# Kernel tuning notes

Hardware: AMD Instinct MI355X
Metric: run time of the kernel (lower is better)

Reference implementation:

```python
import jax, jax.numpy as jnp
import numpy as np

R = 131072   # rays
S = 128      # existing samples per ray (existing_bins has S+1 edges)
N_NEW = 64   # new importance samples per ray
HIST_PAD = 1e-5   # NeuSSampler builds PDFSampler(histogram_padding=1e-5)
EPS = 1e-5


def setup_inputs() -> dict:
    key = jax.random.key(0)
    k1, k2, k3, k4 = jax.random.split(key, 4)
    weights = jax.random.uniform(k1, (R, S, 1), dtype=jnp.float32)
    # existing spacing bins must be sorted in [0,1] along the sample axis
    existing_bins = jnp.sort(jax.random.uniform(k2, (R, S + 1), dtype=jnp.float32), axis=-1)
    nears = 0.05 + 0.5 * jax.random.uniform(k3, (R, 1), dtype=jnp.float32)
    fars = nears + 1.0 + 3.0 * jax.random.uniform(k4, (R, 1), dtype=jnp.float32)
    return {"weights": weights, "existing_bins": existing_bins,
            "nears": nears, "fars": fars, "num_samples": N_NEW}


def reference(weights, existing_bins, nears, fars, num_samples):
    # PDFSampler.generate_ray_samples core (eval mode, include_original=False)
    num_bins = num_samples + 1
    w = weights[..., 0] + HIST_PAD                      # [R, S]
    w_sum = jnp.sum(w, axis=-1, keepdims=True)          # [R, 1]
    padding = jax.nn.relu(EPS - w_sum)
    w = w + padding / w.shape[-1]
    w_sum = w_sum + padding
    pdf = w / w_sum                                     # [R, S]
    cdf = jnp.minimum(jnp.ones_like(pdf), jnp.cumsum(pdf, axis=-1))
    cdf = jnp.concatenate([jnp.zeros_like(cdf[..., :1]), cdf], axis=-1)  # [R, S+1]

    # deterministic mid-bin query points (non-stratified branch)
    u = jnp.linspace(0.0, 1.0 - 1.0 / num_bins, num_bins, dtype=cdf.dtype)
    u = u + 1.0 / (2 * num_bins)
    u = jnp.broadcast_to(u, (*cdf.shape[:-1], num_bins))  # [R, num_bins]

    # inverse-CDF: per-ray binary search + gather + linear interp
    inds = jax.vmap(lambda c, q: jnp.searchsorted(c, q, side='right'))(cdf, u)
    last = existing_bins.shape[-1] - 1
    below = jnp.clip(inds - 1, 0, last)
    above = jnp.clip(inds, 0, last)
    cdf_g0 = jnp.take_along_axis(cdf, below, axis=-1)
    bins_g0 = jnp.take_along_axis(existing_bins, below, axis=-1)
    cdf_g1 = jnp.take_along_axis(cdf, above, axis=-1)
    bins_g1 = jnp.take_along_axis(existing_bins, above, axis=-1)
    t = jnp.clip(jnp.nan_to_num((u - cdf_g0) / (cdf_g1 - cdf_g0), nan=0.0,
                                posinf=0.0, neginf=0.0), 0.0, 1.0)
    bins = bins_g0 + t * (bins_g1 - bins_g0)            # [R, num_bins]
    bins = jax.lax.stop_gradient(bins)                  # torch: bins.detach()

    # spacing_to_euclidean_fn for UniformSampler: x*s_far + (1-x)*s_near
    euclidean_bins = bins * fars + (1.0 - bins) * nears  # [R, num_bins]
    return euclidean_bins
```

## Files before the change

kernel.cpp:

```cpp
#include <hip/hip_runtime.h>


#define DPP_FADD(x, ctrl, rmask)                                             \
    ((x) + __int_as_float(__builtin_amdgcn_update_dpp(                       \
               0, __float_as_int(x), (ctrl), (rmask), 0xf, true)))

__global__ __launch_bounds__(256) void neus_sampler_kernel(
    const float* __restrict__ weights,
    const float* __restrict__ bins_g,
    const float* __restrict__ nears,
    const float* __restrict__ fars,
    float* __restrict__ out,
    int R)
{
    constexpr int S  = 128;
    constexpr int SE = 129;
    constexpr int NB = 65;
    constexpr float HPAD = 1e-5f;

    const int lane = threadIdx.x & 63;
    const int gw   = blockIdx.x * 4 + (threadIdx.x >> 6);
    const int nw   = gridDim.x * 4;

    auto jf = [](float c) -> int {
        int j = (int)ceilf(fmaf(65.0f, c, -0.5f));
        return j < 0 ? 0 : (j > NB ? NB : j);
    };

    float2 W, Bp;
    float  BL, NE, FA;

    int ray = gw;
    if (ray < R) {
        const int ur = __builtin_amdgcn_readfirstlane(ray);
        W = reinterpret_cast<const float2*>(weights + (size_t)ur * S)[lane];
        const float* brow = bins_g + (size_t)ur * SE;
        Bp = reinterpret_cast<const float2*>(brow)[lane];
        BL = brow[S]; NE = nears[ur]; FA = fars[ur];
    }

    while (ray < R) {
        const int nray = ray + nw;
        float2 W2, B2; float BL2, NE2, FA2;
        if (nray < R) {
            const int ur2 = __builtin_amdgcn_readfirstlane(nray);
            W2 = reinterpret_cast<const float2*>(weights + (size_t)ur2 * S)[lane];
            const float* brow2 = bins_g + (size_t)ur2 * SE;
            B2 = reinterpret_cast<const float2*>(brow2)[lane];
            BL2 = brow2[S]; NE2 = nears[ur2]; FA2 = fars[ur2];
        }

        const int ur = __builtin_amdgcn_readfirstlane(ray);
        const float w1 = W.y + HPAD;
        float ps = (W.x + HPAD) + w1;
        ps = DPP_FADD(ps, 0x111, 0xf);
        ps = DPP_FADD(ps, 0x112, 0xf);
        ps = DPP_FADD(ps, 0x114, 0xf);
        ps = DPP_FADD(ps, 0x118, 0xf);
        ps = DPP_FADD(ps, 0x142, 0xa);
        ps = DPP_FADD(ps, 0x143, 0xc);

        const float total = __int_as_float(
            __builtin_amdgcn_readlane(__float_as_int(ps), 63));
        const float padding = fmaxf(1e-5f - total, 0.0f);
        const float padc    = padding * (1.0f / S);
        const float inv     = __builtin_amdgcn_rcpf(total + padding);

        const float c_hi  = fminf(1.0f, fmaf((float)(2*lane+2), padc, ps) * inv);
        const float c_mid = fminf(1.0f, fmaf((float)(2*lane+1), padc, ps - w1) * inv);
        float c_lo = __shfl_up(c_hi, 1, 64);
        if (lane == 0) c_lo = 0.0f;
        float b2 = __shfl_down(Bp.x, 1, 64);
        if (lane == 63) b2 = BL;

        const int j0 = jf(c_lo);
        const int j2 = (lane == 63) ? NB : jf(c_hi);
        int j1 = jf(c_mid);
        j1 = j1 < j0 ? j0 : (j1 > j2 ? j2 : j1);

        const float fmn = FA - NE;
        float* orow = out + (size_t)ur * NB;

        if (j1 > j0) {
            const float r  = __builtin_amdgcn_rcpf(c_mid - c_lo);
            const float dt = r * (1.0f / 65.0f);
            const float bd = Bp.y - Bp.x;
            float t = fmaf((float)(2*j0+1), (1.0f/130.0f), -c_lo) * r;
            for (int j = j0; j < j1; ++j) {
                const float tc = fminf(fmaxf(t, 0.0f), 1.0f);
                orow[j] = fmaf(fmaf(tc, bd, Bp.x), fmn, NE);
                t += dt;
            }
        }
        if (j2 > j1) {
            const float r  = __builtin_amdgcn_rcpf(c_hi - c_mid);
            const float dt = r * (1.0f / 65.0f);
            const float bd = b2 - Bp.y;
            float t = fmaf((float)(2*j1+1), (1.0f/130.0f), -c_mid) * r;
            for (int j = j1; j < j2; ++j) {
                const float tc = fminf(fmaxf(t, 0.0f), 1.0f);
                orow[j] = fmaf(fmaf(tc, bd, Bp.y), fmn, NE);
                t += dt;
            }
        }

        ray = nray;
        W = W2; Bp = B2; BL = BL2; NE = NE2; FA = FA2;
    }
}

extern "C" void kernel_launch(void* const* d_in, const int* in_sizes, int n_in,
                              void* d_out, int out_size, void* d_ws, size_t ws_size,
                              hipStream_t stream) {
    const float* weights = (const float*)d_in[0];
    const float* ebins   = (const float*)d_in[1];
    const float* nears   = (const float*)d_in[2];
    const float* fars    = (const float*)d_in[3];
    float* out = (float*)d_out;
    const int R = in_sizes[0] / 128;
    const int blocks = 2048;
    hipLaunchKernelGGL(neus_sampler_kernel, dim3(blocks), dim3(256), 0, stream,
                       weights, ebins, nears, fars, out, R);
}
```

Measured before the change: 171.4 us.

## Deepen ray prefetch pipeline to three stages and replace shuffles with DPP/readlane

Each wave's software pipeline goes from one ray of prefetch to three rays in flight, so more global loads are outstanding while the scan and interpolation run. The cross-lane shuffles for the previous CDF and the next bin edge become a DPP wave-shift-right and a direct per-lane load of brow[2*lane+2]. Near and far are loaded by two different lanes and broadcast with readlane. The cost is more registers per thread, which could lower occupancy.

```diff
diff --git a/kernel.cpp b/kernel.cpp
--- a/kernel.cpp
+++ b/kernel.cpp
@@ -22,37 +22,32 @@
     const int gw   = blockIdx.x * 4 + (threadIdx.x >> 6);
     const int nw   = gridDim.x * 4;
 
+    struct Stage { float wx, wy, bx, by, b2, nf; };
+
+    auto issue = [&](int r) -> Stage {
+        Stage st;
+        const int ur = __builtin_amdgcn_readfirstlane(r);
+        const float2 w =
+            reinterpret_cast<const float2*>(weights + (size_t)ur * S)[lane];
+        st.wx = w.x; st.wy = w.y;
+        const float* brow = bins_g + (size_t)ur * SE;
+        const float2 b = reinterpret_cast<const float2*>(brow)[lane];
+        st.bx = b.x; st.by = b.y;
+        st.b2 = brow[2 * lane + 2];
+        const float* pa = (lane == 1) ? (fars + ur) : (nears + ur);
+        st.nf = *pa;
+        return st;
+    };
+
     auto jf = [](float c) -> int {
         int j = (int)ceilf(fmaf(65.0f, c, -0.5f));
         return j < 0 ? 0 : (j > NB ? NB : j);
     };
 
-    float2 W, Bp;
-    float  BL, NE, FA;
-
-    int ray = gw;
-    if (ray < R) {
-        const int ur = __builtin_amdgcn_readfirstlane(ray);
-        W = reinterpret_cast<const float2*>(weights + (size_t)ur * S)[lane];
-        const float* brow = bins_g + (size_t)ur * SE;
-        Bp = reinterpret_cast<const float2*>(brow)[lane];
-        BL = brow[S]; NE = nears[ur]; FA = fars[ur];
-    }
-
-    while (ray < R) {
-        const int nray = ray + nw;
-        float2 W2, B2; float BL2, NE2, FA2;
-        if (nray < R) {
-            const int ur2 = __builtin_amdgcn_readfirstlane(nray);
-            W2 = reinterpret_cast<const float2*>(weights + (size_t)ur2 * S)[lane];
-            const float* brow2 = bins_g + (size_t)ur2 * SE;
-            B2 = reinterpret_cast<const float2*>(brow2)[lane];
-            BL2 = brow2[S]; NE2 = nears[ur2]; FA2 = fars[ur2];
-        }
-
-        const int ur = __builtin_amdgcn_readfirstlane(ray);
-        const float w1 = W.y + HPAD;
-        float ps = (W.x + HPAD) + w1;
+    auto compute = [&](const Stage& st, int r) {
+        const int ur = __builtin_amdgcn_readfirstlane(r);
+        const float w1 = st.wy + HPAD;
+        float ps = (st.wx + HPAD) + w1;
         ps = DPP_FADD(ps, 0x111, 0xf);
         ps = DPP_FADD(ps, 0x112, 0xf);
         ps = DPP_FADD(ps, 0x114, 0xf);
@@ -68,44 +63,62 @@
 
         const float c_hi  = fminf(1.0f, fmaf((float)(2*lane+2), padc, ps) * inv);
         const float c_mid = fminf(1.0f, fmaf((float)(2*lane+1), padc, ps - w1) * inv);
-        float c_lo = __shfl_up(c_hi, 1, 64);
-        if (lane == 0) c_lo = 0.0f;
-        float b2 = __shfl_down(Bp.x, 1, 64);
-        if (lane == 63) b2 = BL;
+        const float c_lo = __int_as_float(__builtin_amdgcn_update_dpp(
+            0, __float_as_int(c_hi), 0x138, 0xf, 0xf, true));
+
+        const float ne = __int_as_float(
+            __builtin_amdgcn_readlane(__float_as_int(st.nf), 0));
+        const float fa = __int_as_float(
+            __builtin_amdgcn_readlane(__float_as_int(st.nf), 1));
 
         const int j0 = jf(c_lo);
         const int j2 = (lane == 63) ? NB : jf(c_hi);
         int j1 = jf(c_mid);
         j1 = j1 < j0 ? j0 : (j1 > j2 ? j2 : j1);
 
-        const float fmn = FA - NE;
+        const float fmn = fa - ne;
         float* orow = out + (size_t)ur * NB;
 
         if (j1 > j0) {
-            const float r  = __builtin_amdgcn_rcpf(c_mid - c_lo);
-            const float dt = r * (1.0f / 65.0f);
-            const float bd = Bp.y - Bp.x;
-            float t = fmaf((float)(2*j0+1), (1.0f/130.0f), -c_lo) * r;
+            const float r1 = __builtin_amdgcn_rcpf(c_mid - c_lo);
+            const float dt = r1 * (1.0f / 65.0f);
+            const float bd = st.by - st.bx;
+            float t = fmaf((float)(2*j0+1), (1.0f/130.0f), -c_lo) * r1;
             for (int j = j0; j < j1; ++j) {
                 const float tc = fminf(fmaxf(t, 0.0f), 1.0f);
-                orow[j] = fmaf(fmaf(tc, bd, Bp.x), fmn, NE);
+                orow[j] = fmaf(fmaf(tc, bd, st.bx), fmn, ne);
                 t += dt;
             }
         }
         if (j2 > j1) {
-            const float r  = __builtin_amdgcn_rcpf(c_hi - c_mid);
-            const float dt = r * (1.0f / 65.0f);
-            const float bd = b2 - Bp.y;
-            float t = fmaf((float)(2*j1+1), (1.0f/130.0f), -c_mid) * r;
+            const float r1 = __builtin_amdgcn_rcpf(c_hi - c_mid);
+            const float dt = r1 * (1.0f / 65.0f);
+            const float bd = st.b2 - st.by;
+            float t = fmaf((float)(2*j1+1), (1.0f/130.0f), -c_mid) * r1;
             for (int j = j1; j < j2; ++j) {
                 const float tc = fminf(fmaxf(t, 0.0f), 1.0f);
-                orow[j] = fmaf(fmaf(tc, bd, Bp.y), fmn, NE);
+                orow[j] = fmaf(fmaf(tc, bd, st.by), fmn, ne);
                 t += dt;
             }
         }
+    };
 
-        ray = nray;
-        W = W2; Bp = B2; BL = BL2; NE = NE2; FA = FA2;
+    int ray = gw;
+    if (ray >= R) return;
+    Stage s0, s1, s2;
+    s0 = issue(ray);
+    const int r1i = ray + nw, r2i = ray + 2 * nw;
+    if (r1i < R) s1 = issue(r1i);
+    if (r2i < R) s2 = issue(r2i);
+
+    int nxt = ray + 3 * nw;
+    while (true) {
+        compute(s0, ray);
+        ray += nw;
+        if (ray >= R) break;
+        s0 = s1; s1 = s2;
+        if (nxt < R) s2 = issue(nxt);
+        nxt += nw;
     }
 }
 
```

Measured after the change: 172.8 us. No clear change (+0.8%).
